# Optimization experiments

Measured on AMD Instinct MI355X. Metric: run time of the kernel, lower is better.

The kernel has to match this reference:

```python
import jax, jax.numpy as jnp
import numpy as np

N = 50000
E = 600000
NFEAT = 128
NHID = 128
PAD_N = 60000


def setup_inputs() -> dict:
    key = jax.random.key(0)
    ks = jax.random.split(key, 10)
    x = jax.random.normal(ks[0], (N, NFEAT), dtype=jnp.float32)
    edge_index = jax.random.randint(ks[1], (2, E), 0, N, dtype=jnp.int64)
    pos_idx = jnp.arange(N, dtype=jnp.int64)
    # SAGEConv params: lin_l (applied to mean-aggregated neighbors, with bias),
    # lin_r (applied to root/self features, no bias). Two layers.
    s1 = 1.0 / np.sqrt(NFEAT)
    s2 = 1.0 / np.sqrt(NHID)
    Wl1 = jax.random.uniform(ks[2], (NFEAT, NHID), jnp.float32, -s1, s1)
    Wr1 = jax.random.uniform(ks[3], (NFEAT, NHID), jnp.float32, -s1, s1)
    b1 = jax.random.uniform(ks[4], (NHID,), jnp.float32, -s1, s1)
    Wl2 = jax.random.uniform(ks[5], (NHID, NHID), jnp.float32, -s2, s2)
    Wr2 = jax.random.uniform(ks[6], (NHID, NHID), jnp.float32, -s2, s2)
    b2 = jax.random.uniform(ks[7], (NHID,), jnp.float32, -s2, s2)
    return {"x": x, "edge_index": edge_index, "pos_idx": pos_idx, "pad_n": PAD_N,
            "Wl1": Wl1, "Wr1": Wr1, "b1": b1, "Wl2": Wl2, "Wr2": Wr2, "b2": b2}


def _sage_conv(h, src, dst, Wl, Wr, b):
    # mean aggregation of source features into destination nodes
    msg = h[src]                                              # [E, F]
    agg = jax.ops.segment_sum(msg, dst, num_segments=N)       # [N, F]
    cnt = jax.ops.segment_sum(jnp.ones((dst.shape[0],), h.dtype), dst, num_segments=N)
    agg = agg / jnp.maximum(cnt, 1.0)[:, None]
    return agg @ Wl + h @ Wr + b


def reference(x, edge_index, pos_idx, pad_n, Wl1, Wr1, b1, Wl2, Wr2, b2):
    src, dst = edge_index[0], edge_index[1]
    h = jax.nn.relu(_sage_conv(x, src, dst, Wl1, Wr1, b1))
    # dropout is a no-op in eval mode (training=False)
    h = jax.nn.relu(_sage_conv(h, src, dst, Wl2, Wr2, b2))
    out = jnp.zeros((pad_n, h.shape[1]), h.dtype).at[pos_idx].set(h)
    return out
```

## Files before the change

kernel.cpp:

```cpp
#include <hip/hip_runtime.h>


#define NF 128
#define SCAN_B 256
#define MB 64

typedef _Float16 f16x8 __attribute__((ext_vector_type(8)));
typedef _Float16 f16x4 __attribute__((ext_vector_type(4)));
typedef float f32x4 __attribute__((ext_vector_type(4)));

__device__ __forceinline__ void swizzle_w(const float* __restrict__ Wl,
                                          const float* __restrict__ Wr,
                                          _Float16* __restrict__ Wf, int t) {
    int lane = t & 63;
    int frag = t >> 6;
    int s = frag >> 3, c = frag & 7;
    int n = s * 16 + (lane & 15);
    int kbase = c * 32 + (lane >> 4) * 8;
    f16x8 v;
#pragma unroll
    for (int j = 0; j < 8; ++j) {
        int k = kbase + j;
        float f = (k < NF) ? Wl[k * NF + n] : Wr[(k - NF) * NF + n];
        v[j] = (_Float16)f;
    }
    ((f16x8*)Wf)[frag * 64 + lane] = v;
}

__global__ void init_swz_kernel(float4* __restrict__ tail, int n4tail,
                                int4* __restrict__ deg4, int ndeg4,
                                const float* __restrict__ Wl1, const float* __restrict__ Wr1,
                                _Float16* __restrict__ Wf1,
                                const float* __restrict__ Wl2, const float* __restrict__ Wr2,
                                _Float16* __restrict__ Wf2) {
    int nbt = (n4tail + 255) >> 8;
    int nbd = (ndeg4 + 255) >> 8;
    int b = blockIdx.x;
    if (b < nbt) {
        int i = b * 256 + threadIdx.x;
        if (i < n4tail) tail[i] = make_float4(0.f, 0.f, 0.f, 0.f);
    } else if (b < nbt + nbd) {
        int i = (b - nbt) * 256 + threadIdx.x;
        if (i < ndeg4) deg4[i] = make_int4(0, 0, 0, 0);
    } else if (b < nbt + nbd + 16) {
        swizzle_w(Wl1, Wr1, Wf1, (b - nbt - nbd) * 256 + threadIdx.x);
    } else {
        swizzle_w(Wl2, Wr2, Wf2, (b - nbt - nbd - 16) * 256 + threadIdx.x);
    }
}

__global__ void cvt_hist_kernel(const float4* __restrict__ x4, f16x4* __restrict__ xh4,
                                int n4x,
                                const int* __restrict__ dst, int* __restrict__ deg, int E) {
    int nbc = (n4x + 255) >> 8;
    int b = blockIdx.x;
    if (b < nbc) {
        int i = b * 256 + threadIdx.x;
        if (i < n4x) {
            float4 v = x4[i];
            f16x4 o;
            o[0] = (_Float16)v.x; o[1] = (_Float16)v.y;
            o[2] = (_Float16)v.z; o[3] = (_Float16)v.w;
            xh4[i] = o;
        }
    } else {
        int e = (b - nbc) * 256 + threadIdx.x;
        if (e < E) atomicAdd(&deg[dst[e]], 1);
    }
}

__global__ void alloc_kernel(const int* __restrict__ deg, int* __restrict__ row_start,
                             int* __restrict__ row_end, int* __restrict__ gcur, int Nn) {
    __shared__ int s[SCAN_B];
    __shared__ int sbase;
    int t = threadIdx.x, i = blockIdx.x * SCAN_B + t;
    int v = (i < Nn) ? deg[i] : 0;
    s[t] = v; __syncthreads();
    for (int off = 1; off < SCAN_B; off <<= 1) {
        int add = (t >= off) ? s[t - off] : 0;
        __syncthreads();
        s[t] += add; __syncthreads();
    }
    if (t == SCAN_B - 1) sbase = atomicAdd(gcur, s[t]);
    __syncthreads();
    if (i < Nn) {
        int base = sbase + s[t] - v;
        row_start[i] = base;
        row_end[i]   = base + v;
    }
}

__global__ void fill_kernel(const int* __restrict__ src, const int* __restrict__ dst,
                            const int* __restrict__ row_start,
                            int* __restrict__ deg, int* __restrict__ csr, int E) {
    int e = blockIdx.x * blockDim.x + threadIdx.x;
    if (e < E) {
        int d = dst[e];
        int slot = atomicSub(&deg[d], 1) - 1;
        csr[row_start[d] + slot] = src[e];
    }
}

__global__ __launch_bounds__(256) void gather_mean_kernel(
    const int* __restrict__ csr, const int* __restrict__ row_start,
    const int* __restrict__ row_end,
    const _Float16* __restrict__ H, _Float16* __restrict__ agg, int Nn) {
    int wid = (blockIdx.x * blockDim.x + threadIdx.x) >> 6;
    int sub = (threadIdx.x >> 4) & 3;
    int li  = threadIdx.x & 15;
    int n = wid * 4 + sub;
    if (n >= Nn) return;
    int rs = row_start[n], re = row_end[n];
    const f16x8* Hp = (const f16x8*)H;
    float a[8] = {0.f, 0.f, 0.f, 0.f, 0.f, 0.f, 0.f, 0.f};
    float b[8] = {0.f, 0.f, 0.f, 0.f, 0.f, 0.f, 0.f, 0.f};
    int k = rs;
    for (; k + 4 <= re; k += 4) {
        f16x8 v0 = Hp[(size_t)csr[k] * 16 + li];
        f16x8 v1 = Hp[(size_t)csr[k + 1] * 16 + li];
        f16x8 v2 = Hp[(size_t)csr[k + 2] * 16 + li];
        f16x8 v3 = Hp[(size_t)csr[k + 3] * 16 + li];
#pragma unroll
        for (int j = 0; j < 8; ++j) {
            a[j] += (float)v0[j] + (float)v2[j];
            b[j] += (float)v1[j] + (float)v3[j];
        }
    }
    if (k + 2 <= re) {
        f16x8 v0 = Hp[(size_t)csr[k] * 16 + li];
        f16x8 v1 = Hp[(size_t)csr[k + 1] * 16 + li];
#pragma unroll
        for (int j = 0; j < 8; ++j) { a[j] += (float)v0[j]; b[j] += (float)v1[j]; }
        k += 2;
    }
    if (k < re) {
        f16x8 v0 = Hp[(size_t)csr[k] * 16 + li];
#pragma unroll
        for (int j = 0; j < 8; ++j) a[j] += (float)v0[j];
    }
    float inv = 1.0f / fmaxf((float)(re - rs), 1.0f);
    f16x8 r;
#pragma unroll
    for (int j = 0; j < 8; ++j) r[j] = (_Float16)((a[j] + b[j]) * inv);
    ((f16x8*)agg)[(size_t)n * 16 + li] = r;
}

template <bool LAST>
__global__ __launch_bounds__(256) void gemm_kernel(
    const _Float16* __restrict__ A,
    const _Float16* __restrict__ X,
    const _Float16* __restrict__ Wf,
    const float* __restrict__ bias,
    const int* __restrict__ pos,
    _Float16* __restrict__ outh,
    float* __restrict__ outf,
    int Nn) {
    const int wave = threadIdx.x >> 6;
    const int lane = threadIdx.x & 63;
    const int m0 = blockIdx.x * MB;
    const int mrow = lane & 15, quad = lane >> 4;

    f16x8 bfrag[2][8];
    const f16x8* wfp = (const f16x8*)Wf;
#pragma unroll
    for (int s = 0; s < 2; ++s)
#pragma unroll
        for (int c = 0; c < 8; ++c)
            bfrag[s][c] = wfp[((2 * wave + s) * 8 + c) * 64 + lane];

    f32x4 acc[4][2];
#pragma unroll
    for (int mt = 0; mt < 4; ++mt)
#pragma unroll
        for (int s = 0; s < 2; ++s)
            acc[mt][s] = (f32x4){0.f, 0.f, 0.f, 0.f};

    int nd[4];
#pragma unroll
    for (int mt = 0; mt < 4; ++mt) {
        int n = m0 + mt * 16 + mrow;
        nd[mt] = (n < Nn) ? n : (Nn - 1);
    }

#pragma unroll
    for (int half = 0; half < 2; ++half) {
        const _Float16* __restrict__ src = half ? X : A;
#pragma unroll
        for (int c = 0; c < 4; ++c) {
            int koff = c * 32 + quad * 8;
            int cc = half * 4 + c;
#pragma unroll
            for (int mt = 0; mt < 4; ++mt) {
                f16x8 afrag = *(const f16x8*)(src + (size_t)nd[mt] * NF + koff);
                acc[mt][0] = __builtin_amdgcn_mfma_f32_16x16x32_f16(
                    afrag, bfrag[0][cc], acc[mt][0], 0, 0, 0);
                acc[mt][1] = __builtin_amdgcn_mfma_f32_16x16x32_f16(
                    afrag, bfrag[1][cc], acc[mt][1], 0, 0, 0);
            }
        }
    }

#pragma unroll
    for (int s = 0; s < 2; ++s) {
        int feat = (2 * wave + s) * 16 + mrow;
        float b = bias[feat];
#pragma unroll
        for (int mt = 0; mt < 4; ++mt) {
#pragma unroll
            for (int r = 0; r < 4; ++r) {
                int node = m0 + mt * 16 + quad * 4 + r;
                if (node < Nn) {
                    float v = fmaxf(acc[mt][s][r] + b, 0.f);
                    if (LAST) outf[(size_t)pos[node] * NF + feat] = v;
                    else      outh[(size_t)node * NF + feat] = (_Float16)v;
                }
            }
        }
    }
}

extern "C" void kernel_launch(void* const* d_in, const int* in_sizes, int n_in,
                              void* d_out, int out_size, void* d_ws, size_t ws_size,
                              hipStream_t stream) {
    const float* x   = (const float*)d_in[0];
    const int*   ei  = (const int*)d_in[1];
    const int*   pos = (const int*)d_in[2];
    const float* Wl1 = (const float*)d_in[4];
    const float* Wr1 = (const float*)d_in[5];
    const float* b1  = (const float*)d_in[6];
    const float* Wl2 = (const float*)d_in[7];
    const float* Wr2 = (const float*)d_in[8];
    const float* b2  = (const float*)d_in[9];
    float* out = (float*)d_out;

    const int Nn = in_sizes[0] / NF;
    const int E  = in_sizes[1] / 2;
    const int* src = ei;
    const int* dst = ei + E;
    const int pad_rows = out_size / NF;

    const int degN = (Nn + 3) & ~3;
    _Float16* xh   = (_Float16*)d_ws;
    _Float16* h1h  = xh + (size_t)Nn * NF;
    _Float16* aggh = h1h + (size_t)Nn * NF;
    _Float16* Wf1  = aggh + (size_t)Nn * NF;
    _Float16* Wf2  = Wf1 + 64 * 64 * 8;
    int* deg       = (int*)(Wf2 + 64 * 64 * 8);
    int* gcur      = deg + degN;
    int* row_start = gcur + 4;
    int* row_end   = row_start + Nn;
    int* csr       = row_end + Nn;

    const int ZB = 256;

    int n4tail = (pad_rows - Nn) * NF / 4;
    int ndeg4  = degN / 4 + 1;
    int nbt = (n4tail + ZB - 1) / ZB, nbd = (ndeg4 + ZB - 1) / ZB;
    init_swz_kernel<<<nbt + nbd + 32, ZB, 0, stream>>>(
        (float4*)(out + (size_t)Nn * NF), n4tail, (int4*)deg, ndeg4,
        Wl1, Wr1, Wf1, Wl2, Wr2, Wf2);

    int n4x = Nn * NF / 4;
    int nbc = (n4x + ZB - 1) / ZB;
    cvt_hist_kernel<<<nbc + (E + ZB - 1) / ZB, ZB, 0, stream>>>(
        (const float4*)x, (f16x4*)xh, n4x, dst, deg, E);

    alloc_kernel<<<(Nn + SCAN_B - 1) / SCAN_B, SCAN_B, 0, stream>>>(
        deg, row_start, row_end, gcur, Nn);

    fill_kernel<<<(E + ZB - 1) / ZB, ZB, 0, stream>>>(src, dst, row_start, deg, csr, E);

    const int gblocks = (Nn + 16 - 1) / 16;
    const int mblocks = (Nn + MB - 1) / MB;

    gather_mean_kernel<<<gblocks, ZB, 0, stream>>>(csr, row_start, row_end, xh, aggh, Nn);
    gemm_kernel<false><<<mblocks, 256, 0, stream>>>(aggh, xh, Wf1, b1, nullptr,
                                                    h1h, nullptr, Nn);

    gather_mean_kernel<<<gblocks, ZB, 0, stream>>>(csr, row_start, row_end, h1h, aggh, Nn);
    gemm_kernel<true><<<mblocks, 256, 0, stream>>>(aggh, h1h, Wf2, b2, pos,
                                                   nullptr, out, Nn);
}
```

Measured before the change: 254.2 us.

## Fuse neighbor mean gather with SAGE GEMM via shared-memory tile

Merges the gather-mean kernel and the MFMA GEMM kernel into one per-layer kernel. Each 256-thread block gathers and averages 16 node rows into an LDS tile, then runs the GEMM on that tile plus the self features. This removes the aggregated-feature round trip through global memory and two kernel launches. In exchange, each block now reloads the full swizzled weight fragments for only 16 rows instead of 64, which multiplies weight traffic fourfold.

```diff
diff --git a/kernel.cpp b/kernel.cpp
--- a/kernel.cpp
+++ b/kernel.cpp
@@ -3,7 +3,7 @@
 
 #define NF 128
 #define SCAN_B 256
-#define MB 64
+#define LDA 136
 
 typedef _Float16 f16x8 __attribute__((ext_vector_type(8)));
 typedef _Float16 f16x4 __attribute__((ext_vector_type(4)));
@@ -101,64 +101,64 @@
     }
 }
 
-__global__ __launch_bounds__(256) void gather_mean_kernel(
+template <bool LAST>
+__global__ __launch_bounds__(256) void sage_layer_fused(
     const int* __restrict__ csr, const int* __restrict__ row_start,
     const int* __restrict__ row_end,
-    const _Float16* __restrict__ H, _Float16* __restrict__ agg, int Nn) {
-    int wid = (blockIdx.x * blockDim.x + threadIdx.x) >> 6;
-    int sub = (threadIdx.x >> 4) & 3;
-    int li  = threadIdx.x & 15;
-    int n = wid * 4 + sub;
-    if (n >= Nn) return;
-    int rs = row_start[n], re = row_end[n];
-    const f16x8* Hp = (const f16x8*)H;
-    float a[8] = {0.f, 0.f, 0.f, 0.f, 0.f, 0.f, 0.f, 0.f};
-    float b[8] = {0.f, 0.f, 0.f, 0.f, 0.f, 0.f, 0.f, 0.f};
-    int k = rs;
-    for (; k + 4 <= re; k += 4) {
-        f16x8 v0 = Hp[(size_t)csr[k] * 16 + li];
-        f16x8 v1 = Hp[(size_t)csr[k + 1] * 16 + li];
-        f16x8 v2 = Hp[(size_t)csr[k + 2] * 16 + li];
-        f16x8 v3 = Hp[(size_t)csr[k + 3] * 16 + li];
-#pragma unroll
-        for (int j = 0; j < 8; ++j) {
-            a[j] += (float)v0[j] + (float)v2[j];
-            b[j] += (float)v1[j] + (float)v3[j];
-        }
-    }
-    if (k + 2 <= re) {
-        f16x8 v0 = Hp[(size_t)csr[k] * 16 + li];
-        f16x8 v1 = Hp[(size_t)csr[k + 1] * 16 + li];
-#pragma unroll
-        for (int j = 0; j < 8; ++j) { a[j] += (float)v0[j]; b[j] += (float)v1[j]; }
-        k += 2;
-    }
-    if (k < re) {
-        f16x8 v0 = Hp[(size_t)csr[k] * 16 + li];
-#pragma unroll
-        for (int j = 0; j < 8; ++j) a[j] += (float)v0[j];
-    }
-    float inv = 1.0f / fmaxf((float)(re - rs), 1.0f);
-    f16x8 r;
-#pragma unroll
-    for (int j = 0; j < 8; ++j) r[j] = (_Float16)((a[j] + b[j]) * inv);
-    ((f16x8*)agg)[(size_t)n * 16 + li] = r;
-}
-
-template <bool LAST>
-__global__ __launch_bounds__(256) void gemm_kernel(
-    const _Float16* __restrict__ A,
-    const _Float16* __restrict__ X,
+    const _Float16* __restrict__ H,
     const _Float16* __restrict__ Wf,
     const float* __restrict__ bias,
     const int* __restrict__ pos,
     _Float16* __restrict__ outh,
     float* __restrict__ outf,
     int Nn) {
+    __shared__ _Float16 sA[16][LDA];
+
     const int wave = threadIdx.x >> 6;
     const int lane = threadIdx.x & 63;
-    const int m0 = blockIdx.x * MB;
-    const int mrow = lane & 15, quad = lane >> 4;
+    const int sub  = lane >> 4;
+    const int li   = lane & 15;
+    const int m0 = blockIdx.x * 16;
+
+    {
+        int n = m0 + wave * 4 + sub;
+        float a[8] = {0.f, 0.f, 0.f, 0.f, 0.f, 0.f, 0.f, 0.f};
+        float b[8] = {0.f, 0.f, 0.f, 0.f, 0.f, 0.f, 0.f, 0.f};
+        float inv = 1.0f;
+        if (n < Nn) {
+            int rs = row_start[n], re = row_end[n];
+            const f16x8* Hp = (const f16x8*)H;
+            int k = rs;
+            for (; k + 4 <= re; k += 4) {
+                f16x8 v0 = Hp[(size_t)csr[k] * 16 + li];
+                f16x8 v1 = Hp[(size_t)csr[k + 1] * 16 + li];
+                f16x8 v2 = Hp[(size_t)csr[k + 2] * 16 + li];
+                f16x8 v3 = Hp[(size_t)csr[k + 3] * 16 + li];
+#pragma unroll
+                for (int j = 0; j < 8; ++j) {
+                    a[j] += (float)v0[j] + (float)v2[j];
+                    b[j] += (float)v1[j] + (float)v3[j];
+                }
+            }
+            if (k + 2 <= re) {
+                f16x8 v0 = Hp[(size_t)csr[k] * 16 + li];
+                f16x8 v1 = Hp[(size_t)csr[k + 1] * 16 + li];
+#pragma unroll
+                for (int j = 0; j < 8; ++j) { a[j] += (float)v0[j]; b[j] += (float)v1[j]; }
+                k += 2;
+            }
+            if (k < re) {
+                f16x8 v0 = Hp[(size_t)csr[k] * 16 + li];
+#pragma unroll
+                for (int j = 0; j < 8; ++j) a[j] += (float)v0[j];
+            }
+            inv = 1.0f / fmaxf((float)(re - rs), 1.0f);
+        }
+        f16x8 r;
+#pragma unroll
+        for (int j = 0; j < 8; ++j) r[j] = (_Float16)((a[j] + b[j]) * inv);
+        *(f16x8*)&sA[wave * 4 + sub][li * 8] = r;
+    }
 
     f16x8 bfrag[2][8];
     const f16x8* wfp = (const f16x8*)Wf;
@@ -168,52 +168,38 @@
         for (int c = 0; c < 8; ++c)
             bfrag[s][c] = wfp[((2 * wave + s) * 8 + c) * 64 + lane];
 
-    f32x4 acc[4][2];
-#pragma unroll
-    for (int mt = 0; mt < 4; ++mt)
-#pragma unroll
-        for (int s = 0; s < 2; ++s)
-            acc[mt][s] = (f32x4){0.f, 0.f, 0.f, 0.f};
-
-    int nd[4];
-#pragma unroll
-    for (int mt = 0; mt < 4; ++mt) {
-        int n = m0 + mt * 16 + mrow;
-        nd[mt] = (n < Nn) ? n : (Nn - 1);
-    }
-
-#pragma unroll
-    for (int half = 0; half < 2; ++half) {
-        const _Float16* __restrict__ src = half ? X : A;
+    __syncthreads();
+
+    f32x4 acc[2] = {(f32x4){0.f, 0.f, 0.f, 0.f}, (f32x4){0.f, 0.f, 0.f, 0.f}};
+
+#pragma unroll
+    for (int c = 0; c < 4; ++c) {
+        f16x8 af = *(const f16x8*)&sA[li][c * 32 + sub * 8];
+        acc[0] = __builtin_amdgcn_mfma_f32_16x16x32_f16(af, bfrag[0][c], acc[0], 0, 0, 0);
+        acc[1] = __builtin_amdgcn_mfma_f32_16x16x32_f16(af, bfrag[1][c], acc[1], 0, 0, 0);
+    }
+    {
+        int nd = m0 + li; if (nd >= Nn) nd = Nn - 1;
+        const _Float16* xrow = H + (size_t)nd * NF;
 #pragma unroll
         for (int c = 0; c < 4; ++c) {
-            int koff = c * 32 + quad * 8;
-            int cc = half * 4 + c;
-#pragma unroll
-            for (int mt = 0; mt < 4; ++mt) {
-                f16x8 afrag = *(const f16x8*)(src + (size_t)nd[mt] * NF + koff);
-                acc[mt][0] = __builtin_amdgcn_mfma_f32_16x16x32_f16(
-                    afrag, bfrag[0][cc], acc[mt][0], 0, 0, 0);
-                acc[mt][1] = __builtin_amdgcn_mfma_f32_16x16x32_f16(
-                    afrag, bfrag[1][cc], acc[mt][1], 0, 0, 0);
-            }
+            f16x8 af = *(const f16x8*)(xrow + c * 32 + sub * 8);
+            acc[0] = __builtin_amdgcn_mfma_f32_16x16x32_f16(af, bfrag[0][4 + c], acc[0], 0, 0, 0);
+            acc[1] = __builtin_amdgcn_mfma_f32_16x16x32_f16(af, bfrag[1][4 + c], acc[1], 0, 0, 0);
         }
     }
 
 #pragma unroll
     for (int s = 0; s < 2; ++s) {
-        int feat = (2 * wave + s) * 16 + mrow;
-        float b = bias[feat];
-#pragma unroll
-        for (int mt = 0; mt < 4; ++mt) {
-#pragma unroll
-            for (int r = 0; r < 4; ++r) {
-                int node = m0 + mt * 16 + quad * 4 + r;
-                if (node < Nn) {
-                    float v = fmaxf(acc[mt][s][r] + b, 0.f);
-                    if (LAST) outf[(size_t)pos[node] * NF + feat] = v;
-                    else      outh[(size_t)node * NF + feat] = (_Float16)v;
-                }
+        int feat = (2 * wave + s) * 16 + li;
+        float bv = bias[feat];
+#pragma unroll
+        for (int r = 0; r < 4; ++r) {
+            int node = m0 + sub * 4 + r;
+            if (node < Nn) {
+                float v = fmaxf(acc[s][r] + bv, 0.f);
+                if (LAST) outf[(size_t)pos[node] * NF + feat] = v;
+                else      outh[(size_t)node * NF + feat] = (_Float16)v;
             }
         }
     }
@@ -242,8 +228,7 @@
     const int degN = (Nn + 3) & ~3;
     _Float16* xh   = (_Float16*)d_ws;
     _Float16* h1h  = xh + (size_t)Nn * NF;
-    _Float16* aggh = h1h + (size_t)Nn * NF;
-    _Float16* Wf1  = aggh + (size_t)Nn * NF;
+    _Float16* Wf1  = h1h + (size_t)Nn * NF;
     _Float16* Wf2  = Wf1 + 64 * 64 * 8;
     int* deg       = (int*)(Wf2 + 64 * 64 * 8);
     int* gcur      = deg + degN;
@@ -270,14 +255,9 @@
 
     fill_kernel<<<(E + ZB - 1) / ZB, ZB, 0, stream>>>(src, dst, row_start, deg, csr, E);
 
-    const int gblocks = (Nn + 16 - 1) / 16;
-    const int mblocks = (Nn + MB - 1) / MB;
-
-    gather_mean_kernel<<<gblocks, ZB, 0, stream>>>(csr, row_start, row_end, xh, aggh, Nn);
-    gemm_kernel<false><<<mblocks, 256, 0, stream>>>(aggh, xh, Wf1, b1, nullptr,
-                                                    h1h, nullptr, Nn);
-
-    gather_mean_kernel<<<gblocks, ZB, 0, stream>>>(csr, row_start, row_end, h1h, aggh, Nn);
-    gemm_kernel<true><<<mblocks, 256, 0, stream>>>(aggh, h1h, Wf2, b2, pos,
-                                                   nullptr, out, Nn);
-}
+    const int fblocks = (Nn + 15) / 16;
+    sage_layer_fused<false><<<fblocks, ZB, 0, stream>>>(
+        csr, row_start, row_end, xh, Wf1, b1, nullptr, h1h, nullptr, Nn);
+    sage_layer_fused<true><<<fblocks, ZB, 0, stream>>>(
+        csr, row_start, row_end, h1h, Wf2, b2, pos, nullptr, out, Nn);
+}
```

Result: faster. 241.4 us (-5.0%).
